# Kernel tuning notes

Measured on AMD Instinct MI355X. Metric: run time of the kernel, lower is better.

## Reference

```python
import math
import jax, jax.numpy as jnp
import numpy as np

B, S, H = 8, 2048, 1024
NH = 1
DH = H // NH          # head dim == hidden since NH=1 (required by module's math)
DT = 64               # distance_type


def setup_inputs() -> dict:
    key = jax.random.key(0)
    ks = jax.random.split(key, 10)
    hidden_states = jax.random.normal(ks[0], (B, S, H), dtype=jnp.float32)
    attention_mask = jnp.zeros((B, 1, 1, S), dtype=jnp.float32)
    word_word_relation = jax.random.randint(ks[1], (B, S, S), 0, DT, dtype=jnp.int32)
    init = 0.02
    Wq = jax.random.normal(ks[2], (H, H), dtype=jnp.float32) * init
    bq = jnp.zeros((H,), dtype=jnp.float32)
    Wk = jax.random.normal(ks[3], (H, H), dtype=jnp.float32) * init
    bk = jnp.zeros((H,), dtype=jnp.float32)
    Wv = jax.random.normal(ks[4], (H, H), dtype=jnp.float32) * init
    bv = jnp.zeros((H,), dtype=jnp.float32)
    dist_emb = jax.random.normal(ks[5], (DT, H), dtype=jnp.float32) * init
    dist_emb = dist_emb.at[0].set(0.0)  # padding_idx=0
    return {
        "hidden_states": hidden_states,
        "attention_mask": attention_mask,
        "word_word_relation": word_word_relation,
        "Wq": Wq, "bq": bq, "Wk": Wk, "bk": bk, "Wv": Wv, "bv": bv,
        "dist_emb": dist_emb,
    }


def reference(hidden_states, attention_mask, word_word_relation,
              Wq, bq, Wk, bk, Wv, bv, dist_emb):
    b, s, h = hidden_states.shape
    def heads(x):  # [b,s,h] -> [b,nh,s,dh]
        return x.reshape(b, s, NH, DH).transpose(0, 2, 1, 3)
    q = heads(hidden_states @ Wq.T + bq)
    k = heads(hidden_states @ Wk.T + bk)
    v = heads(hidden_states @ Wv.T + bv)

    scores = jnp.einsum('bhqd,bhkd->bhqk', q, k)                 # [b,nh,s,s]
    word_dot_distance = jnp.einsum('bhqd,td->bhqt', q, dist_emb) # [b,nh,s,DT]

    idx = word_word_relation[:, None, :, :]                      # [b,1,s,s]
    bias = jnp.take_along_axis(word_dot_distance, idx, axis=3)
    mask_out = (word_word_relation == 1)[:, None].astype(scores.dtype)
    bias = bias * mask_out

    scores = (scores + bias) / math.sqrt(DH) + attention_mask
    probs = jax.nn.softmax(scores, axis=-1)
    ctx = jnp.einsum('bhqk,bhkd->bhqd', probs, v)
    ctx = ctx.transpose(0, 2, 1, 3).reshape(b, s, h)
    return ctx
```

## Files before the change

### kernel.cpp

```cpp
#include <hip/hip_runtime.h>

typedef unsigned short u16;
typedef __bf16 bf16x8 __attribute__((ext_vector_type(8)));
typedef u16 u16x8 __attribute__((ext_vector_type(8)));
typedef float f32x4 __attribute__((ext_vector_type(4)));

#define S_LEN 2048
#define H_LEN 1024

__device__ __forceinline__ u16 f2b(float f) {
  unsigned u = __float_as_uint(f);
  return (u16)((u + 0x7FFFu + ((u >> 16) & 1u)) >> 16);
}
__device__ __forceinline__ float b2f(u16 h) { return __uint_as_float(((unsigned)h) << 16); }

#define GLOAD16(gp, lp)                                   \
  __builtin_amdgcn_global_load_lds(                       \
      (__attribute__((address_space(1))) void*)(gp),      \
      (__attribute__((address_space(3))) void*)(lp), 16, 0, 0)

#define FENCE() asm volatile("" ::: "memory")
#define PBAR()                           \
  do {                                   \
    FENCE();                             \
    __builtin_amdgcn_s_barrier();        \
    FENCE();                             \
  } while (0)
#define WAIT_LGKM0()                                        \
  do {                                                      \
    asm volatile("s_waitcnt lgkmcnt(0)" ::: "memory");      \
    __builtin_amdgcn_sched_barrier(0);                      \
  } while (0)
#define WAIT_VM(n) asm volatile("s_waitcnt vmcnt(" #n ")" ::: "memory")

__device__ __forceinline__ f32x4 MM(bf16x8 a, bf16x8 b, f32x4 c) {
  return __builtin_amdgcn_mfma_f32_16x16x32_bf16(a, b, c, 0, 0, 0);
}

__global__ __launch_bounds__(256) void prep_kernel(
    const float* __restrict__ X, const float* __restrict__ Wq,
    const float* __restrict__ Wk, const float* __restrict__ Wv,
    const float* __restrict__ bq, const float* __restrict__ bk,
    const float* __restrict__ bv, const float* __restrict__ dist,
    const int* __restrict__ rel,
    u16* __restrict__ Xbf, u16* __restrict__ Wbf, float* __restrict__ b_all,
    u16* __restrict__ de1, unsigned* __restrict__ bits, float* __restrict__ d1) {
  size_t tid = (size_t)blockIdx.x * blockDim.x + threadIdx.x;
  size_t nth = (size_t)gridDim.x * blockDim.x;
  for (size_t i = tid; i < 4194304u; i += nth) {
    float4 v = ((const float4*)X)[i];
    ushort4 o; o.x = f2b(v.x); o.y = f2b(v.y); o.z = f2b(v.z); o.w = f2b(v.w);
    ((ushort4*)Xbf)[i] = o;
  }
  for (size_t i = tid; i < 786432u; i += nth) {
    int which = (int)(i >> 18);
    size_t off = i & 262143u;
    const float4* src = (const float4*)(which == 0 ? Wq : (which == 1 ? Wk : Wv));
    float4 v = src[off];
    ushort4 o; o.x = f2b(v.x); o.y = f2b(v.y); o.z = f2b(v.z); o.w = f2b(v.w);
    ((ushort4*)Wbf)[i] = o;
  }
  const int4* r4 = (const int4*)rel;
  for (size_t wi = tid; wi < 1048576u; wi += nth) {
    const int4* s = r4 + wi * 8;
    unsigned m = 0;
#pragma unroll
    for (int u = 0; u < 8; ++u) {
      int4 v = s[u];
      m |= (unsigned)(v.x == 1) << (u * 4 + 0);
      m |= (unsigned)(v.y == 1) << (u * 4 + 1);
      m |= (unsigned)(v.z == 1) << (u * 4 + 2);
      m |= (unsigned)(v.w == 1) << (u * 4 + 3);
    }
    bits[wi] = m;
  }
  for (size_t i = tid; i < 256u; i += nth) {
    float4 v = ((const float4*)(dist + H_LEN))[i];
    ushort4 o; o.x = f2b(v.x); o.y = f2b(v.y); o.z = f2b(v.z); o.w = f2b(v.w);
    ((ushort4*)de1)[i] = o;
  }
  for (size_t i = tid; i < 3072u; i += nth)
    b_all[i] = (i < 1024) ? bq[i] : (i < 2048 ? bk[i - 1024] : bv[i - 2048]);
  for (size_t i = tid; i < 32768u; i += nth) d1[i] = 0.f;
}

struct GArgs {
  const u16* A; const u16* B;
  long long sA, sB;
  int ldA, ldB, K;
  u16 *Qo, *Ko, *Vo; const float* b_all; const u16* de1; float* d1;
  const unsigned* relbits; const float* mask; u16* P; float* denom;
  float* outp;
};

template <int EPI>
__global__ __launch_bounds__(512, 2) void gemm256(GArgs g) {
  int bx, by, bz;
  {
    const int lin = blockIdx.x;
    if constexpr (EPI == 0) {
      const int wg = (lin & 7) * 96 + (lin >> 3);
      by = wg / 12; bx = wg % 12; bz = 0;
    } else if constexpr (EPI == 1) {
      const int wg = (lin & 7) * 64 + (lin >> 3);
      bz = wg >> 6; by = (wg >> 3) & 7; bx = wg & 7;
    } else {
      const int wg = (lin & 7) * 32 + (lin >> 3);
      bz = wg >> 5; by = (wg >> 2) & 7; bx = wg & 3;
    }
  }
  const u16* Abase = g.A + (size_t)bz * g.sA;
  const u16* Bbase = g.B + (size_t)bz * g.sB;
  const int m0 = by * 256, n0 = bx * 256;

  __shared__ u16 smem[65536];

  const int tid = threadIdx.x;
  const int lane = tid & 63, w = tid >> 6;
  const int wm = w >> 2, wn = w & 3;
  const int l15 = lane & 15, quad = lane >> 4;

  f32x4 acc[8][4];
  const f32x4 zero = {0.f, 0.f, 0.f, 0.f};
#pragma unroll
  for (int a = 0; a < 8; ++a)
#pragma unroll
    for (int b = 0; b < 4; ++b) acc[a][b] = zero;

  const u16* gA[4]; const u16* gB[4]; int qoff[4];
#pragma unroll
  for (int r = 0; r < 4; ++r) {
    const int q = r * 512 + tid;
    const int row = q >> 3, ch = q & 7;
    const int chS = ch ^ (row & 7);
    gA[r] = Abase + (size_t)(m0 + row) * g.ldA + chS * 8;
    gB[r] = Bbase + (size_t)(n0 + row) * g.ldB + chS * 8;
    qoff[r] = q * 8;
  }

  auto stage = [&](int boff2, int kt) {
#pragma unroll
    for (int r = 0; r < 4; ++r) GLOAD16(gA[r] + kt, &smem[boff2 + qoff[r]]);
#pragma unroll
    for (int r = 0; r < 4; ++r) GLOAD16(gB[r] + kt, &smem[boff2 + 16384 + qoff[r]]);
  };

  const int NT = g.K >> 6;

  stage(0, 0);
  stage(32768, 64);
  WAIT_VM(8);
  PBAR();

  bf16x8 af0[4][2], af1[4][2], bf0[2][2], bf1[2][2];

  for (int t = 0; t < NT; ++t) {
    const int boff = (t & 1) << 15;
    const u16* Ab = smem + boff;
    const u16* Bb = smem + boff + 16384;

#pragma unroll
    for (int mt = 0; mt < 4; ++mt) {
      const int row = wm * 128 + mt * 16 + l15;
      const int base = row * 64, rx = row & 7;
      af0[mt][0] = *(const bf16x8*)&Ab[base + ((quad ^ rx) << 3)];
      af0[mt][1] = *(const bf16x8*)&Ab[base + (((quad + 4) ^ rx) << 3)];
    }
#pragma unroll
    for (int nt = 0; nt < 2; ++nt) {
      const int row = wn * 64 + nt * 16 + l15;
      const int base = row * 64, rx = row & 7;
      bf0[nt][0] = *(const bf16x8*)&Bb[base + ((quad ^ rx) << 3)];
      bf0[nt][1] = *(const bf16x8*)&Bb[base + (((quad + 4) ^ rx) << 3)];
    }
#pragma unroll
    for (int nt = 0; nt < 2; ++nt) {
      const int row = wn * 64 + (nt + 2) * 16 + l15;
      const int base = row * 64, rx = row & 7;
      bf1[nt][0] = *(const bf16x8*)&Bb[base + ((quad ^ rx) << 3)];
      bf1[nt][1] = *(const bf16x8*)&Bb[base + (((quad + 4) ^ rx) << 3)];
    }
#pragma unroll
    for (int mt = 0; mt < 4; ++mt) {
      const int row = wm * 128 + (mt + 4) * 16 + l15;
      const int base = row * 64, rx = row & 7;
      af1[mt][0] = *(const bf16x8*)&Ab[base + ((quad ^ rx) << 3)];
      af1[mt][1] = *(const bf16x8*)&Ab[base + (((quad + 4) ^ rx) << 3)];
    }

    __builtin_amdgcn_s_setprio(1);
#pragma unroll
    for (int mt = 0; mt < 4; ++mt)
#pragma unroll
      for (int nt = 0; nt < 2; ++nt)
        acc[mt][nt] = MM(af0[mt][0], bf0[nt][0], acc[mt][nt]);
#pragma unroll
    for (int mt = 0; mt < 4; ++mt)
#pragma unroll
      for (int nt = 0; nt < 2; ++nt)
        acc[mt][nt] = MM(af0[mt][1], bf0[nt][1], acc[mt][nt]);
    __builtin_amdgcn_s_setprio(0);

    __builtin_amdgcn_s_setprio(1);
#pragma unroll
    for (int mt = 0; mt < 4; ++mt)
#pragma unroll
      for (int nt = 0; nt < 2; ++nt)
        acc[mt][nt + 2] = MM(af0[mt][0], bf1[nt][0], acc[mt][nt + 2]);
#pragma unroll
    for (int mt = 0; mt < 4; ++mt)
#pragma unroll
      for (int nt = 0; nt < 2; ++nt)
        acc[mt][nt + 2] = MM(af0[mt][1], bf1[nt][1], acc[mt][nt + 2]);
    __builtin_amdgcn_s_setprio(0);

    __builtin_amdgcn_s_setprio(1);
#pragma unroll
    for (int mt = 0; mt < 4; ++mt)
#pragma unroll
      for (int nt = 0; nt < 2; ++nt)
        acc[mt + 4][nt] = MM(af1[mt][0], bf0[nt][0], acc[mt + 4][nt]);
#pragma unroll
    for (int mt = 0; mt < 4; ++mt)
#pragma unroll
      for (int nt = 0; nt < 2; ++nt)
        acc[mt + 4][nt] = MM(af1[mt][1], bf0[nt][1], acc[mt + 4][nt]);
    __builtin_amdgcn_s_setprio(0);

    WAIT_LGKM0();
    PBAR();
    if (t + 2 < NT) stage(boff, (t + 2) << 6);

    __builtin_amdgcn_s_setprio(1);
#pragma unroll
    for (int mt = 0; mt < 4; ++mt)
#pragma unroll
      for (int nt = 0; nt < 2; ++nt)
        acc[mt + 4][nt + 2] = MM(af1[mt][0], bf1[nt][0], acc[mt + 4][nt + 2]);
#pragma unroll
    for (int mt = 0; mt < 4; ++mt)
#pragma unroll
      for (int nt = 0; nt < 2; ++nt)
        acc[mt + 4][nt + 2] = MM(af1[mt][1], bf1[nt][1], acc[mt + 4][nt + 2]);
    __builtin_amdgcn_s_setprio(0);

    if (t + 2 < NT) {
      WAIT_VM(8);
    } else if (t + 1 < NT) {
      WAIT_VM(0);
    }
    PBAR();
  }

  const int nbase = n0 + wn * 64;

  if constexpr (EPI == 0) {
    const int which = n0 >> 10;
    const int nl0 = n0 & 1023;
    float bv4[4], dw[4];
#pragma unroll
    for (int nt = 0; nt < 4; ++nt) {
      const int col = wn * 64 + nt * 16 + l15;
      bv4[nt] = g.b_all[n0 + col];
      dw[nt] = (which == 0) ? b2f(g.de1[nl0 + col]) : 0.f;
    }
#pragma unroll
    for (int mt = 0; mt < 8; ++mt)
#pragma unroll
      for (int r = 0; r < 4; ++r) {
        const int row = wm * 128 + mt * 16 + quad * 4 + r;
        float part = 0.f;
#pragma unroll
        for (int nt = 0; nt < 4; ++nt) {
          const float v = acc[mt][nt][r] + bv4[nt];
          part += v * dw[nt];
          const int col = wn * 64 + nt * 16 + l15;
          const int chS = (col >> 3) ^ (row & 31);
          smem[row * 256 + chS * 8 + (col & 7)] = f2b(v);
        }
        if (which == 0) {
          part += __shfl_xor(part, 1);
          part += __shfl_xor(part, 2);
          part += __shfl_xor(part, 4);
          part += __shfl_xor(part, 8);
          if (l15 == 0) atomicAdd(&g.d1[m0 + row], part);
        }
      }
    __syncthreads();
    u16* dstbuf = which == 0 ? g.Qo : (which == 1 ? g.Ko : g.Vo);
#pragma unroll
    for (int p = 0; p < 16; ++p) {
      const int flat = p * 512 + tid;
      const int row = flat >> 5, chunk = flat & 31;
      const int chS = chunk ^ (row & 31);
      u16x8 v = *(const u16x8*)&smem[row * 256 + chS * 8];
      *(u16x8*)(dstbuf + (size_t)(m0 + row) * H_LEN + nl0 + chunk * 8) = v;
    }
  }

  if constexpr (EPI == 1) {
    float mk[4];
#pragma unroll
    for (int nt = 0; nt < 4; ++nt) mk[nt] = g.mask[bz * S_LEN + nbase + nt * 16 + l15];
    const size_t bSS = (size_t)bz * S_LEN * S_LEN;
    const int wbase = (n0 + wn * 64) >> 5;
#pragma unroll
    for (int mt = 0; mt < 8; ++mt)
#pragma unroll
      for (int r = 0; r < 4; ++r) {
        const int row = wm * 128 + mt * 16 + quad * 4 + r;
        const int gi = bz * S_LEN + m0 + row;
        const float d1v = g.d1[gi] * 0.03125f;
        const unsigned w0 = g.relbits[(size_t)gi * 64 + wbase];
        const unsigned w1 = g.relbits[(size_t)gi * 64 + wbase + 1];
        float dsum = 0.f;
#pragma unroll
        for (int nt = 0; nt < 4; ++nt) {
          const unsigned word = (nt & 2) ? w1 : w0;
          const int pos = (nt * 16 + l15) & 31;
          const float bias = ((word >> pos) & 1) ? d1v : 0.f;
          const float logit = acc[mt][nt][r] * 0.03125f + bias + mk[nt];
          const float pv = __expf(logit);
          const u16 pb = f2b(pv);
          dsum += b2f(pb);
          const int col = wn * 64 + nt * 16 + l15;
          const int chS = (col >> 3) ^ (row & 31);
          smem[row * 256 + chS * 8 + (col & 7)] = pb;
        }
        dsum += __shfl_xor(dsum, 1);
        dsum += __shfl_xor(dsum, 2);
        dsum += __shfl_xor(dsum, 4);
        dsum += __shfl_xor(dsum, 8);
        if (l15 == 0) atomicAdd(&g.denom[gi], dsum);
      }
    __syncthreads();
#pragma unroll
    for (int p = 0; p < 16; ++p) {
      const int flat = p * 512 + tid;
      const int row = flat >> 5, chunk = flat & 31;
      const int chS = chunk ^ (row & 31);
      u16x8 v = *(const u16x8*)&smem[row * 256 + chS * 8];
      *(u16x8*)(g.P + bSS + (size_t)(m0 + row) * S_LEN + n0 + chunk * 8) = v;
    }
  }

  if constexpr (EPI == 2) {
    const size_t ob = (size_t)bz * S_LEN * H_LEN;
#pragma unroll
    for (int mt = 0; mt < 8; ++mt)
#pragma unroll
      for (int r = 0; r < 4; ++r) {
        const int row = wm * 128 + mt * 16 + quad * 4 + r;
        const float inv = 1.0f / g.denom[bz * S_LEN + m0 + row];
        const size_t rowo = ob + (size_t)(m0 + row) * H_LEN;
#pragma unroll
        for (int nt = 0; nt < 4; ++nt)
          g.outp[rowo + nbase + nt * 16 + l15] = acc[mt][nt][r] * inv;
      }
  }
}

__global__ __launch_bounds__(256) void transpose_v(const u16* __restrict__ V,
                                                   u16* __restrict__ Vt) {
  const int b = blockIdx.z;
  const int j0 = blockIdx.x * 64;
  const int d0 = blockIdx.y * 64;
  __shared__ u16 t[64][72];
  const int tid = threadIdx.x;
  const int tr = tid >> 4;
  const int tc = (tid & 15) * 4;
#pragma unroll
  for (int p = 0; p < 4; ++p) {
    const int jl = p * 16 + tr;
    const u16* src = V + ((size_t)b * S_LEN + (j0 + jl)) * H_LEN + d0 + tc;
    ushort4 v = *(const ushort4*)src;
    t[jl][tc + 0] = v.x; t[jl][tc + 1] = v.y; t[jl][tc + 2] = v.z; t[jl][tc + 3] = v.w;
  }
  __syncthreads();
#pragma unroll
  for (int p = 0; p < 4; ++p) {
    const int dl = p * 16 + tr;
    ushort4 v;
    v.x = t[tc + 0][dl]; v.y = t[tc + 1][dl]; v.z = t[tc + 2][dl]; v.w = t[tc + 3][dl];
    *(ushort4*)(Vt + ((size_t)b * H_LEN + (d0 + dl)) * S_LEN + j0 + tc) = v;
  }
}

extern "C" void kernel_launch(void* const* d_in, const int* in_sizes, int n_in,
                              void* d_out, int out_size, void* d_ws, size_t ws_size,
                              hipStream_t stream) {
  (void)in_sizes; (void)n_in; (void)out_size; (void)ws_size;
  const float* X    = (const float*)d_in[0];
  const float* mask = (const float*)d_in[1];
  const int*   rel  = (const int*)d_in[2];
  const float* Wq   = (const float*)d_in[3];
  const float* bq   = (const float*)d_in[4];
  const float* Wk   = (const float*)d_in[5];
  const float* bk   = (const float*)d_in[6];
  const float* Wv   = (const float*)d_in[7];
  const float* bv   = (const float*)d_in[8];
  const float* dist = (const float*)d_in[9];
  float* out = (float*)d_out;

  char* p = (char*)d_ws;
  u16* Xbf = (u16*)p;      p += (size_t)16384 * 1024 * 2;
  u16* Wbf = (u16*)p;      p += (size_t)3072 * 1024 * 2;
  float* b_all = (float*)p; p += 3072 * 4;
  u16* de1 = (u16*)p;      p += 4096;
  u16* Qb = (u16*)p;       p += (size_t)16384 * 1024 * 2;
  u16* Kb = (u16*)p;       p += (size_t)16384 * 1024 * 2;
  u16* Vb = (u16*)p;       p += (size_t)16384 * 1024 * 2;
  u16* Vt = (u16*)p;       p += (size_t)16384 * 1024 * 2;
  float* d1 = (float*)p;   p += 16384 * 4;
  float* denom = (float*)p; p += 16384 * 4;
  unsigned* relbits = (unsigned*)p; p += (size_t)1048576 * 4;
  u16* P = (u16*)p;        p += (size_t)8 * 2048 * 2048 * 2;

  prep_kernel<<<1024, 256, 0, stream>>>(X, Wq, Wk, Wv, bq, bk, bv, dist, rel,
                                        Xbf, Wbf, b_all, de1, relbits, d1);

  GArgs g0 = {};
  g0.A = Xbf; g0.B = Wbf; g0.sA = 0; g0.sB = 0;
  g0.ldA = 1024; g0.ldB = 1024; g0.K = 1024;
  g0.Qo = Qb; g0.Ko = Kb; g0.Vo = Vb; g0.b_all = b_all; g0.de1 = de1; g0.d1 = d1;
  gemm256<0><<<dim3(768, 1, 1), dim3(512, 1, 1), 0, stream>>>(g0);

  transpose_v<<<dim3(32, 16, 8), dim3(256, 1, 1), 0, stream>>>(Vb, Vt);

  GArgs g1 = {};
  g1.A = Qb; g1.B = Kb; g1.sA = 2048LL * 1024; g1.sB = 2048LL * 1024;
  g1.ldA = 1024; g1.ldB = 1024; g1.K = 1024;
  g1.relbits = relbits; g1.d1 = d1; g1.mask = mask; g1.P = P; g1.denom = denom;
  gemm256<1><<<dim3(512, 1, 1), dim3(512, 1, 1), 0, stream>>>(g1);

  GArgs g2 = {};
  g2.A = P; g2.B = Vt; g2.sA = 2048LL * 2048; g2.sB = 1024LL * 2048;
  g2.ldA = 2048; g2.ldB = 2048; g2.K = 2048;
  g2.denom = denom; g2.outp = out;
  gemm256<2><<<dim3(256, 1, 1), dim3(512, 1, 1), 0, stream>>>(g2);
}
```

Baseline: 592.3 us.

## Interleave global-to-LDS prefetch quarters with MFMA phases in GEMM main loop

Splits each tile's global-to-LDS staging into four quarter-loads and issues them between the four MFMA compute phases, with barriers and LDS waits around each phase. Before, the next tile was staged in one burst of eight loads before the last phase. This spreads memory traffic across the iteration and overlaps it with matrix work, in a ping-pong style schedule. It adds more barriers per iteration and changes the double-buffer ordering, which could cost synchronization overhead or create hazards.

Result: no change. 594.0 us (+0.3%).

```diff
diff --git a/kernel.cpp b/kernel.cpp
--- a/kernel.cpp
+++ b/kernel.cpp
@@ -138,18 +138,25 @@
     qoff[r] = q * 8;
   }
 
-  auto stage = [&](int boff2, int kt) {
-#pragma unroll
-    for (int r = 0; r < 4; ++r) GLOAD16(gA[r] + kt, &smem[boff2 + qoff[r]]);
-#pragma unroll
-    for (int r = 0; r < 4; ++r) GLOAD16(gB[r] + kt, &smem[boff2 + 16384 + qoff[r]]);
+  const int NT = g.K >> 6;
+
+  auto stage2 = [&](int tile, int pr) {
+    if (tile >= NT) return;
+    const int boff2 = (tile & 1) << 15;
+    const int kt = tile << 6;
+    if (pr < 2) {
+      GLOAD16(gA[2 * pr] + kt,     &smem[boff2 + qoff[2 * pr]]);
+      GLOAD16(gA[2 * pr + 1] + kt, &smem[boff2 + qoff[2 * pr + 1]]);
+    } else {
+      const int r = 2 * (pr - 2);
+      GLOAD16(gB[r] + kt,     &smem[boff2 + 16384 + qoff[r]]);
+      GLOAD16(gB[r + 1] + kt, &smem[boff2 + 16384 + qoff[r + 1]]);
+    }
   };
 
-  const int NT = g.K >> 6;
-
-  stage(0, 0);
-  stage(32768, 64);
-  WAIT_VM(8);
+  stage2(0, 0); stage2(0, 1); stage2(0, 2); stage2(0, 3);
+  stage2(1, 0);
+  if (1 < NT) { WAIT_VM(2); } else { WAIT_VM(0); }
   PBAR();
 
   bf16x8 af0[4][2], af1[4][2], bf0[2][2], bf1[2][2];
@@ -173,6 +180,21 @@
       bf0[nt][0] = *(const bf16x8*)&Bb[base + ((quad ^ rx) << 3)];
       bf0[nt][1] = *(const bf16x8*)&Bb[base + (((quad + 4) ^ rx) << 3)];
     }
+    stage2(t + 1, 1);
+    asm volatile("s_waitcnt lgkmcnt(8)" ::: "memory");
+    PBAR();
+    WAIT_LGKM0();
+    __builtin_amdgcn_s_setprio(1);
+#pragma unroll
+    for (int mt = 0; mt < 4; ++mt)
+#pragma unroll
+      for (int nt = 0; nt < 2; ++nt) {
+        acc[mt][nt] = MM(af0[mt][0], bf0[nt][0], acc[mt][nt]);
+        acc[mt][nt] = MM(af0[mt][1], bf0[nt][1], acc[mt][nt]);
+      }
+    __builtin_amdgcn_s_setprio(0);
+    PBAR();
+
 #pragma unroll
     for (int nt = 0; nt < 2; ++nt) {
       const int row = wn * 64 + (nt + 2) * 16 + l15;
@@ -180,6 +202,20 @@
       bf1[nt][0] = *(const bf16x8*)&Bb[base + ((quad ^ rx) << 3)];
       bf1[nt][1] = *(const bf16x8*)&Bb[base + (((quad + 4) ^ rx) << 3)];
     }
+    stage2(t + 1, 2);
+    PBAR();
+    WAIT_LGKM0();
+    __builtin_amdgcn_s_setprio(1);
+#pragma unroll
+    for (int mt = 0; mt < 4; ++mt)
+#pragma unroll
+      for (int nt = 0; nt < 2; ++nt) {
+        acc[mt][nt + 2] = MM(af0[mt][0], bf1[nt][0], acc[mt][nt + 2]);
+        acc[mt][nt + 2] = MM(af0[mt][1], bf1[nt][1], acc[mt][nt + 2]);
+      }
+    __builtin_amdgcn_s_setprio(0);
+    PBAR();
+
 #pragma unroll
     for (int mt = 0; mt < 4; ++mt) {
       const int row = wm * 128 + (mt + 4) * 16 + l15;
@@ -187,65 +223,34 @@
       af1[mt][0] = *(const bf16x8*)&Ab[base + ((quad ^ rx) << 3)];
       af1[mt][1] = *(const bf16x8*)&Ab[base + (((quad + 4) ^ rx) << 3)];
     }
-
+    stage2(t + 1, 3);
+    PBAR();
+    WAIT_LGKM0();
     __builtin_amdgcn_s_setprio(1);
 #pragma unroll
     for (int mt = 0; mt < 4; ++mt)
 #pragma unroll
-      for (int nt = 0; nt < 2; ++nt)
-        acc[mt][nt] = MM(af0[mt][0], bf0[nt][0], acc[mt][nt]);
+      for (int nt = 0; nt < 2; ++nt) {
+        acc[mt + 4][nt] = MM(af1[mt][0], bf0[nt][0], acc[mt + 4][nt]);
+        acc[mt + 4][nt] = MM(af1[mt][1], bf0[nt][1], acc[mt + 4][nt]);
+      }
+    __builtin_amdgcn_s_setprio(0);
+    PBAR();
+
+    stage2(t + 2, 0);
+    PBAR();
+    WAIT_LGKM0();
+    __builtin_amdgcn_s_setprio(1);
 #pragma unroll
     for (int mt = 0; mt < 4; ++mt)
 #pragma unroll
-      for (int nt = 0; nt < 2; ++nt)
-        acc[mt][nt] = MM(af0[mt][1], bf0[nt][1], acc[mt][nt]);
+      for (int nt = 0; nt < 2; ++nt) {
+        acc[mt + 4][nt + 2] = MM(af1[mt][0], bf1[nt][0], acc[mt + 4][nt + 2]);
+        acc[mt + 4][nt + 2] = MM(af1[mt][1], bf1[nt][1], acc[mt + 4][nt + 2]);
+      }
     __builtin_amdgcn_s_setprio(0);
-
-    __builtin_amdgcn_s_setprio(1);
-#pragma unroll
-    for (int mt = 0; mt < 4; ++mt)
-#pragma unroll
-      for (int nt = 0; nt < 2; ++nt)
-        acc[mt][nt + 2] = MM(af0[mt][0], bf1[nt][0], acc[mt][nt + 2]);
-#pragma unroll
-    for (int mt = 0; mt < 4; ++mt)
-#pragma unroll
-      for (int nt = 0; nt < 2; ++nt)
-        acc[mt][nt + 2] = MM(af0[mt][1], bf1[nt][1], acc[mt][nt + 2]);
-    __builtin_amdgcn_s_setprio(0);
-
-    __builtin_amdgcn_s_setprio(1);
-#pragma unroll
-    for (int mt = 0; mt < 4; ++mt)
-#pragma unroll
-      for (int nt = 0; nt < 2; ++nt)
-        acc[mt + 4][nt] = MM(af1[mt][0], bf0[nt][0], acc[mt + 4][nt]);
-#pragma unroll
-    for (int mt = 0; mt < 4; ++mt)
-#pragma unroll
-      for (int nt = 0; nt < 2; ++nt)
-        acc[mt + 4][nt] = MM(af1[mt][1], bf0[nt][1], acc[mt + 4][nt]);
-    __builtin_amdgcn_s_setprio(0);
-
-    WAIT_LGKM0();
-    PBAR();
-    if (t + 2 < NT) stage(boff, (t + 2) << 6);
-
-    __builtin_amdgcn_s_setprio(1);
-#pragma unroll
-    for (int mt = 0; mt < 4; ++mt)
-#pragma unroll
-      for (int nt = 0; nt < 2; ++nt)
-        acc[mt + 4][nt + 2] = MM(af1[mt][0], bf1[nt][0], acc[mt + 4][nt + 2]);
-#pragma unroll
-    for (int mt = 0; mt < 4; ++mt)
-#pragma unroll
-      for (int nt = 0; nt < 2; ++nt)
-        acc[mt + 4][nt + 2] = MM(af1[mt][1], bf1[nt][1], acc[mt + 4][nt + 2]);
-    __builtin_amdgcn_s_setprio(0);
-
     if (t + 2 < NT) {
-      WAIT_VM(8);
+      WAIT_VM(2);
     } else if (t + 1 < NT) {
       WAIT_VM(0);
     }
```
